# Kernel tuning notes

Hardware: AMD Instinct MI355X
Metric: run time of the kernel (lower is better)

## Reference

```python
import jax, jax.numpy as jnp
import numpy as np

N_PLACE = 100000
N_TRANS = 100000
E = 1000000
F_IN = 128
F_OUT = 64
H = 4
D = F_OUT // H
NEG_SLOPE = 0.2
EPS = 1e-16


def setup_inputs() -> dict:
    key = jax.random.key(0)
    ks = jax.random.split(key, 24)

    def rn(i, shape, s=1.0):
        return jax.random.normal(ks[i], shape, jnp.float32) * s

    def ei(i):
        k1, k2 = jax.random.split(ks[i])
        src = jax.random.randint(k1, (E,), 0, N_PLACE)
        dst = jax.random.randint(k2, (E,), 0, N_PLACE)
        return jnp.stack([src, dst]).astype(jnp.int32)

    return dict(
        x_place=rn(0, (N_PLACE, F_IN)),
        x_trans=rn(1, (N_TRANS, F_IN)),
        W_place=rn(2, (F_IN, F_OUT), 0.1),
        b_place=jnp.zeros((F_OUT,), jnp.float32),
        W_trans=rn(3, (F_IN, F_OUT), 0.1),
        b_trans=jnp.zeros((F_OUT,), jnp.float32),
        as_pt=rn(4, (H, D), 0.1), ad_pt=rn(5, (H, D), 0.1),
        as_tp=rn(6, (H, D), 0.1), ad_tp=rn(7, (H, D), 0.1),
        as_pp=rn(8, (H, D), 0.1), ad_pp=rn(9, (H, D), 0.1),
        as_tt=rn(10, (H, D), 0.1), ad_tt=rn(11, (H, D), 0.1),
        q=rn(12, (F_OUT,), 0.1),
        kW=rn(13, (F_OUT, F_OUT), 0.1),
        kb=jnp.zeros((F_OUT,), jnp.float32),
        ei_pt=ei(14), ei_tp=ei(15), ei_pp=ei(16), ei_tt=ei(17),
    )


def _rel(x_src, x_dst, ei, a_src, a_dst, n_dst):
    # Per-relation GAT-style attention (HANConv inner step).
    # x_src: [N_src, H, D], x_dst: [N_dst, H, D], ei: [2, E]
    src, dst = ei[0], ei[1]
    al_s = jnp.einsum('nhd,hd->nh', x_src, a_src)  # [N_src, H]
    al_d = jnp.einsum('nhd,hd->nh', x_dst, a_dst)  # [N_dst, H]
    alpha = jax.nn.leaky_relu(al_s[src] + al_d[dst], NEG_SLOPE)  # [E, H]
    # segment softmax over incoming edges of each dst node
    m = jax.ops.segment_max(alpha, dst, num_segments=n_dst)  # [N_dst, H]
    e = jnp.exp(alpha - m[dst])
    s = jax.ops.segment_sum(e, dst, num_segments=n_dst)
    a = e / (s[dst] + EPS)  # [E, H]
    out = jax.ops.segment_sum(x_src[src] * a[:, :, None], dst, num_segments=n_dst)
    return jax.nn.relu(out.reshape(n_dst, H * D))


def _group(outs, q, kW, kb):
    # HANConv semantic attention across relations targeting one node type.
    out = jnp.stack(outs)  # [R, N, F]
    score = jnp.einsum('f,rf->r', q, jnp.tanh(out @ kW + kb).mean(axis=1))  # [R]
    attn = jax.nn.softmax(score)
    return jnp.einsum('r,rnf->nf', attn, out)


def reference(x_place, x_trans, W_place, b_place, W_trans, b_trans,
              as_pt, ad_pt, as_tp, ad_tp, as_pp, ad_pp, as_tt, ad_tt,
              q, kW, kb, ei_pt, ei_tp, ei_pp, ei_tt):
    hp = (x_place @ W_place + b_place).reshape(N_PLACE, H, D)
    ht = (x_trans @ W_trans + b_trans).reshape(N_TRANS, H, D)
    out_t_pt = _rel(hp, ht, ei_pt, as_pt, ad_pt, N_TRANS)
    out_t_tt = _rel(ht, ht, ei_tt, as_tt, ad_tt, N_TRANS)
    out_p_tp = _rel(ht, hp, ei_tp, as_tp, ad_tp, N_PLACE)
    out_p_pp = _rel(hp, hp, ei_pp, as_pp, ad_pp, N_PLACE)
    out_place = _group([out_p_tp, out_p_pp], q, kW, kb)
    out_trans = _group([out_t_pt, out_t_tt], q, kW, kb)
    return out_place, out_trans
```

## Files before the change

kernel.cpp:

```cpp
#include <hip/hip_runtime.h>
#include <hip/hip_bf16.h>

#define NN 100000
#define NE 1000000
#define FI 128
#define FO 64
#define NB 196
#define CAP 8192
#define RELSTRIDE (256 * CAP)
#define TILE 4096
#define PROJ_T 512
#define PLACE_BLOCKS 128
#define ALB 128

typedef unsigned short u16;
typedef unsigned int u32;
typedef __attribute__((ext_vector_type(8))) short short8t;
typedef __attribute__((ext_vector_type(4))) float float4t;

__device__ __forceinline__ float bf2f(u16 u) {
    return __uint_as_float(((u32)u) << 16);
}
__device__ __forceinline__ u16 f2bf(float f) {
    __hip_bfloat16 h = __float2bfloat16(f);
    return *(u16*)&h;
}

__global__ __launch_bounds__(256) void init_kernel(int* __restrict__ bcursor,
                                                   float* __restrict__ mean_acc)
{
    const int rel = blockIdx.x;
    const int tid = threadIdx.x;
    bcursor[rel * 256 + tid] = tid * CAP;
    if (tid < 64) mean_acc[rel * 64 + tid] = 0.f;
}

__global__ __launch_bounds__(256) void phase1_kernel(
    const float* __restrict__ x_p, const float* __restrict__ W_p, const float* __restrict__ b_p,
    const float* __restrict__ x_t, const float* __restrict__ W_t, const float* __restrict__ b_t,
    u16* __restrict__ hb_place, u16* __restrict__ hb_trans,
    const int* __restrict__ ei_pt, const int* __restrict__ ei_tt,
    const int* __restrict__ ei_tp, const int* __restrict__ ei_pp,
    int* __restrict__ bcursor, u32* __restrict__ packed)
{
    __shared__ int smem[512];
    const int bid = blockIdx.x;
    const int tid = threadIdx.x;

    if (bid < 2 * PROJ_T) {
        const int ty = (bid >= PROJ_T);
        const float* __restrict__ x = ty ? x_t : x_p;
        const float* __restrict__ W = ty ? W_t : W_p;
        const float* __restrict__ b = ty ? b_t : b_p;
        u16* __restrict__ hout = ty ? hb_trans : hb_place;

        const int lane = tid & 63;
        const int wv   = tid >> 6;
        const int g    = lane >> 4;
        const int lo   = lane & 15;
        const int wid  = ((bid & (PROJ_T - 1)) << 2) | wv;

        short8t wf[4][4];
#pragma unroll
        for (int s = 0; s < 4; ++s)
#pragma unroll
            for (int t = 0; t < 4; ++t)
#pragma unroll
                for (int j = 0; j < 8; ++j)
                    wf[s][t][j] = (short)f2bf(W[(s * 32 + g * 8 + j) * FO + t * 16 + lo]);

        float bias[4];
#pragma unroll
        for (int t = 0; t < 4; ++t) bias[t] = b[t * 16 + lo];

        for (int tile = wid; tile < NN / 16; tile += 2048) {
            const int n0 = tile * 16;
            float4t acc[4];
#pragma unroll
            for (int t = 0; t < 4; ++t) { acc[t][0] = 0.f; acc[t][1] = 0.f; acc[t][2] = 0.f; acc[t][3] = 0.f; }

#pragma unroll
            for (int s = 0; s < 4; ++s) {
                const float* __restrict__ xr = x + (size_t)(n0 + lo) * FI + s * 32 + g * 8;
                const float4 u = *(const float4*)xr;
                const float4 v = *(const float4*)(xr + 4);
                short8t af;
                af[0] = (short)f2bf(u.x); af[1] = (short)f2bf(u.y);
                af[2] = (short)f2bf(u.z); af[3] = (short)f2bf(u.w);
                af[4] = (short)f2bf(v.x); af[5] = (short)f2bf(v.y);
                af[6] = (short)f2bf(v.z); af[7] = (short)f2bf(v.w);
#pragma unroll
                for (int t = 0; t < 4; ++t)
                    acc[t] = __builtin_amdgcn_mfma_f32_16x16x32_bf16(af, wf[s][t], acc[t], 0, 0, 0);
            }

#pragma unroll
            for (int t = 0; t < 4; ++t)
#pragma unroll
                for (int j = 0; j < 4; ++j)
                    hout[(size_t)(n0 + g * 4 + j) * FO + t * 16 + lo] = f2bf(acc[t][j] + bias[t]);
        }
    } else {
        const int pb = bid - 2 * PROJ_T;
        const int rel = pb >> 7;
        const int bx  = pb & 127;
        const int* ei = (rel == 0) ? ei_pt : (rel == 1) ? ei_tt : (rel == 2) ? ei_tp : ei_pp;
        u32* pk = packed + (size_t)rel * RELSTRIDE;

        int* lh = smem;
        int* lb = smem + 256;

        const int ntiles = (NE + TILE - 1) / TILE;
        for (int tile = bx; tile < ntiles; tile += PLACE_BLOCKS) {
            const int t0 = tile * TILE;
            lh[tid] = 0;
            __syncthreads();

            int d[TILE / 256];
#pragma unroll
            for (int i = 0; i < TILE / 256; ++i) {
                const int idx = t0 + i * 256 + tid;
                d[i] = (idx < NE) ? ei[NE + idx] : -1;
                if (d[i] >= 0) atomicAdd(&lh[d[i] >> 9], 1);
            }
            __syncthreads();
            if (lh[tid]) lb[tid] = atomicAdd(&bcursor[rel * 256 + tid], lh[tid]);
            __syncthreads();
#pragma unroll
            for (int i = 0; i < TILE / 256; ++i) {
                const int idx = t0 + i * 256 + tid;
                if (d[i] >= 0) {
                    const int src = ei[idx];
                    const int slot = atomicAdd(&lb[d[i] >> 9], 1);
                    pk[slot] = ((u32)(d[i] & 511) << 17) | (u32)src;
                }
            }
            __syncthreads();
        }
    }
}

__global__ __launch_bounds__(256) void csr_build_al(
    const u32* __restrict__ packed, const int* __restrict__ bcursor,
    int2* __restrict__ ofp, int* __restrict__ perm,
    const u16* __restrict__ hb_place, const u16* __restrict__ hb_trans,
    const float* __restrict__ as_pt, const float* __restrict__ as_pp,
    const float* __restrict__ ad_tp, const float* __restrict__ ad_pp,
    const float* __restrict__ as_tp, const float* __restrict__ as_tt,
    const float* __restrict__ ad_pt, const float* __restrict__ ad_tt,
    float* __restrict__ al_place, float* __restrict__ al_trans)
{
    const int by = blockIdx.y;
    const int bx = blockIdx.x;
    const int tid = threadIdx.x;

    if (bx < NB) {
        const int rel = by;
        const int b = bx;
        const int base = b * CAP;
        const int cnt  = bcursor[rel * 256 + b] - base;
        const u32* pk = packed + (size_t)rel * RELSTRIDE + base;
        int2* of = ofp + (size_t)rel * NN;
        int* pm = perm + (size_t)rel * RELSTRIDE;

        __shared__ int h[512];
        __shared__ int cur[512];
        h[tid] = 0; h[tid + 256] = 0;
        __syncthreads();
        for (int i = tid; i < cnt; i += 256)
            atomicAdd(&h[pk[i] >> 17], 1);
        __syncthreads();
        const int o0 = h[tid], o1 = h[tid + 256];
        for (int off = 1; off < 512; off <<= 1) {
            const int a0 = (tid >= off) ? h[tid - off] : 0;
            const int a1 = (tid + 256 >= off) ? h[tid + 256 - off] : 0;
            __syncthreads();
            h[tid] += a0; h[tid + 256] += a1;
            __syncthreads();
        }
        const int e0 = base + h[tid] - o0;
        const int e1 = base + h[tid + 256] - o1;
        const int gd0 = b * 512 + tid;
        const int gd1 = gd0 + 256;
        if (gd0 < NN) of[gd0] = make_int2(e0, e0 + o0);
        if (gd1 < NN) of[gd1] = make_int2(e1, e1 + o1);
        cur[tid] = e0; cur[tid + 256] = e1;
        __syncthreads();
        for (int i = tid; i < cnt; i += 256) {
            const u32 e = pk[i];
            const int slot = atomicAdd(&cur[e >> 17], 1);
            pm[slot] = (int)(e & 0x1FFFFu);
        }
    } else {
        const int ab = bx - NB;
        const int type = by >> 1;
        const int part = by & 1;
        const u16* hb = type ? hb_trans : hb_place;
        float* al = type ? al_trans : al_place;
        const float* a0 = type ? as_tp : as_pt;
        const float* a1 = type ? as_tt : as_pp;
        const float* a2 = type ? ad_pt : ad_tp;
        const float* a3 = type ? ad_tt : ad_pp;

        const int lane = tid & 63;
        const int wv   = tid >> 6;
        const int head = lane >> 4;
        const float av0 = a0[lane];
        const float av1 = a1[lane];
        const float av2 = a2[lane];
        const float av3 = a3[lane];

        const int HN = NN / 2;
        const int nw = ALB * 4;
        for (int n = part * HN + ab * 4 + wv; n < (part + 1) * HN; n += nw) {
            const float hv = bf2f(hb[(size_t)n * FO + lane]);
            float p0 = hv * av0, p1 = hv * av1, p2 = hv * av2, p3 = hv * av3;
#pragma unroll
            for (int off = 1; off < 16; off <<= 1) {
                p0 += __shfl_xor(p0, off);
                p1 += __shfl_xor(p1, off);
                p2 += __shfl_xor(p2, off);
                p3 += __shfl_xor(p3, off);
            }
            if ((lane & 15) == 0) {
                al[0 * NN * 4 + n * 4 + head] = p0;
                al[1 * NN * 4 + n * 4 + head] = p1;
                al[2 * NN * 4 + n * 4 + head] = p2;
                al[3 * NN * 4 + n * 4 + head] = p3;
            }
        }
    }
}

#define EDGE4(pm_, als_, hb_, cc, advh_, num_, den_, head_, lane_)                                  \
    {                                                                                               \
        const int s0 = pm_[cc], s1 = pm_[cc + 1], s2 = pm_[cc + 2], s3 = pm_[cc + 3];               \
        const float4 v0 = *(const float4*)(als_ + (size_t)s0 * 4);                                  \
        const float4 v1 = *(const float4*)(als_ + (size_t)s1 * 4);                                  \
        const float4 v2 = *(const float4*)(als_ + (size_t)s2 * 4);                                  \
        const float4 v3 = *(const float4*)(als_ + (size_t)s3 * 4);                                  \
        float a0 = ((head_ == 0) ? v0.x : (head_ == 1) ? v0.y : (head_ == 2) ? v0.z : v0.w) + advh_;\
        float a1 = ((head_ == 0) ? v1.x : (head_ == 1) ? v1.y : (head_ == 2) ? v1.z : v1.w) + advh_;\
        float a2 = ((head_ == 0) ? v2.x : (head_ == 1) ? v2.y : (head_ == 2) ? v2.z : v2.w) + advh_;\
        float a3 = ((head_ == 0) ? v3.x : (head_ == 1) ? v3.y : (head_ == 2) ? v3.z : v3.w) + advh_;\
        a0 = a0 > 0.f ? a0 : 0.2f * a0;                                                             \
        a1 = a1 > 0.f ? a1 : 0.2f * a1;                                                             \
        a2 = a2 > 0.f ? a2 : 0.2f * a2;                                                             \
        a3 = a3 > 0.f ? a3 : 0.2f * a3;                                                             \
        const float e0 = __expf(a0), e1 = __expf(a1), e2 = __expf(a2), e3 = __expf(a3);             \
        const float h0 = bf2f(hb_[(size_t)s0 * FO + lane_]);                                        \
        const float h1 = bf2f(hb_[(size_t)s1 * FO + lane_]);                                        \
        const float h2 = bf2f(hb_[(size_t)s2 * FO + lane_]);                                        \
        const float h3 = bf2f(hb_[(size_t)s3 * FO + lane_]);                                        \
        num_ = fmaf(h0, e0, num_);                                                                  \
        num_ = fmaf(h1, e1, num_);                                                                  \
        num_ = fmaf(h2, e2, num_);                                                                  \
        num_ = fmaf(h3, e3, num_);                                                                  \
        den_ += (e0 + e1) + (e2 + e3);                                                              \
    }

#define EDGE1(pm_, als_, hb_, cc, advh_, num_, den_, head_, lane_)                                  \
    {                                                                                               \
        const int s0 = pm_[cc];                                                                     \
        const float4 v0 = *(const float4*)(als_ + (size_t)s0 * 4);                                  \
        float a0 = ((head_ == 0) ? v0.x : (head_ == 1) ? v0.y : (head_ == 2) ? v0.z : v0.w) + advh_;\
        a0 = a0 > 0.f ? a0 : 0.2f * a0;                                                             \
        const float e0 = __expf(a0);                                                                \
        const float h0 = bf2f(hb_[(size_t)s0 * FO + lane_]);                                        \
        num_ = fmaf(h0, e0, num_);                                                                  \
        den_ += e0;                                                                                 \
    }

__global__ __launch_bounds__(256) void acc_kernel(
    const u16* __restrict__ hb_place, const u16* __restrict__ hb_trans,
    const float* __restrict__ al_place, const float* __restrict__ al_trans,
    const int2* __restrict__ ofp, const int* __restrict__ perm,
    u16* __restrict__ outb)
{
    const int rel = blockIdx.y;
    const u16* hb; const float* als; const float* ald;
    if (rel == 0)      { hb = hb_place; als = al_place + 0 * NN * 4; ald = al_trans + 2 * NN * 4; }
    else if (rel == 1) { hb = hb_trans; als = al_trans + 1 * NN * 4; ald = al_trans + 3 * NN * 4; }
    else if (rel == 2) { hb = hb_trans; als = al_trans + 0 * NN * 4; ald = al_place + 2 * NN * 4; }
    else               { hb = hb_place; als = al_place + 1 * NN * 4; ald = al_place + 3 * NN * 4; }
    const int2* of = ofp + (size_t)rel * NN;
    const int* pm = perm + (size_t)rel * RELSTRIDE;
    u16* ob = outb + (size_t)rel * NN * FO;

    const int lane = threadIdx.x & 63;
    const int wid  = threadIdx.x >> 6;
    const int head = lane >> 4;

    const int gw = blockIdx.x * 4 + wid;
    const int nw = gridDim.x * 4;
    for (int n = gw; n < NN; n += 2 * nw) {
        const int n2 = n + nw;
        const int nu = __builtin_amdgcn_readfirstlane(n);
        const int2 be = of[nu];
        int c1 = be.x;
        const int end1 = be.y;
        const float advh1 = ald[nu * 4 + head];
        float num1 = 0.f, den1 = 0.f;

        if (n2 < NN) {
            const int nu2 = __builtin_amdgcn_readfirstlane(n2);
            const int2 be2 = of[nu2];
            int c2 = be2.x;
            const int end2 = be2.y;
            const float advh2 = ald[nu2 * 4 + head];
            float num2 = 0.f, den2 = 0.f;

            while (c1 + 4 <= end1 && c2 + 4 <= end2) {
                EDGE4(pm, als, hb, c1, advh1, num1, den1, head, lane);
                EDGE4(pm, als, hb, c2, advh2, num2, den2, head, lane);
                c1 += 4; c2 += 4;
            }
            for (; c1 + 4 <= end1; c1 += 4) EDGE4(pm, als, hb, c1, advh1, num1, den1, head, lane);
            for (; c1 < end1; ++c1)         EDGE1(pm, als, hb, c1, advh1, num1, den1, head, lane);
            for (; c2 + 4 <= end2; c2 += 4) EDGE4(pm, als, hb, c2, advh2, num2, den2, head, lane);
            for (; c2 < end2; ++c2)         EDGE1(pm, als, hb, c2, advh2, num2, den2, head, lane);

            const float outv1 = fmaxf(num1 / (den1 + 1e-16f), 0.f);
            const float outv2 = fmaxf(num2 / (den2 + 1e-16f), 0.f);
            ob[(size_t)nu * FO + lane]  = f2bf(outv1);
            ob[(size_t)nu2 * FO + lane] = f2bf(outv2);
        } else {
            for (; c1 + 4 <= end1; c1 += 4) EDGE4(pm, als, hb, c1, advh1, num1, den1, head, lane);
            for (; c1 < end1; ++c1)         EDGE1(pm, als, hb, c1, advh1, num1, den1, head, lane);
            const float outv1 = fmaxf(num1 / (den1 + 1e-16f), 0.f);
            ob[(size_t)nu * FO + lane] = f2bf(outv1);
        }
    }
}

__global__ __launch_bounds__(256) void sem_kernel(
    const u16* __restrict__ outb, const float* __restrict__ kW, const float* __restrict__ kb,
    float* __restrict__ mean_acc)
{
    const int rel = blockIdx.y;
    const u16* ob = outb + (size_t)rel * NN * FO;
    const int QN = NN / 4;

    const int lane = threadIdx.x & 63;
    const int wid  = threadIdx.x >> 6;

    float kwc[FO];
#pragma unroll
    for (int k = 0; k < FO; ++k) kwc[k] = kW[k * FO + lane];
    const float kbv = kb[lane];

    float ts = 0.f;
    const int gw = blockIdx.x * 4 + wid;
    const int nw = gridDim.x * 4;
    for (int n = gw; n < QN; n += nw) {
        const int r0 = __builtin_amdgcn_readfirstlane(n);
        const int r1 = r0 + QN;
        const int r2 = r0 + 2 * QN;
        const int r3 = r0 + 3 * QN;
        const u32* w0 = (const u32*)(ob + (size_t)r0 * FO);
        const u32* w1 = (const u32*)(ob + (size_t)r1 * FO);
        const u32* w2 = (const u32*)(ob + (size_t)r2 * FO);
        const u32* w3 = (const u32*)(ob + (size_t)r3 * FO);
        float y0 = kbv, y1 = kbv, y2 = kbv, y3 = kbv;
#pragma unroll
        for (int i = 0; i < 32; ++i) {
            const u32 a = w0[i], b = w1[i], c = w2[i], d = w3[i];
            y0 = fmaf(__uint_as_float(a << 16),         kwc[2 * i],     y0);
            y0 = fmaf(__uint_as_float(a & 0xffff0000u), kwc[2 * i + 1], y0);
            y1 = fmaf(__uint_as_float(b << 16),         kwc[2 * i],     y1);
            y1 = fmaf(__uint_as_float(b & 0xffff0000u), kwc[2 * i + 1], y1);
            y2 = fmaf(__uint_as_float(c << 16),         kwc[2 * i],     y2);
            y2 = fmaf(__uint_as_float(c & 0xffff0000u), kwc[2 * i + 1], y2);
            y3 = fmaf(__uint_as_float(d << 16),         kwc[2 * i],     y3);
            y3 = fmaf(__uint_as_float(d & 0xffff0000u), kwc[2 * i + 1], y3);
        }
        ts += (tanhf(y0) + tanhf(y1)) + (tanhf(y2) + tanhf(y3));
    }

    __shared__ float red[4][64];
    red[wid][lane] = ts;
    __syncthreads();
    if (wid == 0) {
        const float sum = red[0][lane] + red[1][lane] + red[2][lane] + red[3][lane];
        unsafeAtomicAdd(&mean_acc[rel * 64 + lane], sum);
    }
}

__global__ __launch_bounds__(256) void combine_kernel(
    const u16* __restrict__ outb, const float* __restrict__ mean_acc,
    const float* __restrict__ q, float* __restrict__ out)
{
    const int lane = threadIdx.x & 63;
    const int type = blockIdx.y;
    const int r0i = (type == 0) ? 2 : 0;

    const float qv = q[lane];
    float s0 = qv * mean_acc[r0i * 64 + lane] * (1.0f / (float)NN);
    float s1 = qv * mean_acc[(r0i + 1) * 64 + lane] * (1.0f / (float)NN);
#pragma unroll
    for (int off = 1; off < 64; off <<= 1) {
        s0 += __shfl_xor(s0, off);
        s1 += __shfl_xor(s1, off);
    }
    const float m = fmaxf(s0, s1);
    const float e0 = expf(s0 - m), e1 = expf(s1 - m);
    const float a0 = e0 / (e0 + e1);
    const float a1 = e1 / (e0 + e1);

    const ushort4* o0 = (const ushort4*)(outb + (size_t)r0i * NN * FO);
    const ushort4* o1 = (const ushort4*)(outb + (size_t)(r0i + 1) * NN * FO);
    float4* dst = (float4*)(out + (size_t)type * NN * FO);
    const int n4 = NN * FO / 4;
    const int stride = gridDim.x * 256;
    for (int i = blockIdx.x * 256 + threadIdx.x; i < n4; i += stride) {
        const ushort4 u = o0[i];
        const ushort4 w = o1[i];
        float4 r;
        r.x = a0 * bf2f(u.x) + a1 * bf2f(w.x);
        r.y = a0 * bf2f(u.y) + a1 * bf2f(w.y);
        r.z = a0 * bf2f(u.z) + a1 * bf2f(w.z);
        r.w = a0 * bf2f(u.w) + a1 * bf2f(w.w);
        dst[i] = r;
    }
}

extern "C" void kernel_launch(void* const* d_in, const int* in_sizes, int n_in,
                              void* d_out, int out_size, void* d_ws, size_t ws_size,
                              hipStream_t stream)
{
    const float* x_place = (const float*)d_in[0];
    const float* x_trans = (const float*)d_in[1];
    const float* W_place = (const float*)d_in[2];
    const float* b_place = (const float*)d_in[3];
    const float* W_trans = (const float*)d_in[4];
    const float* b_trans = (const float*)d_in[5];
    const float* as_pt = (const float*)d_in[6];
    const float* ad_pt = (const float*)d_in[7];
    const float* as_tp = (const float*)d_in[8];
    const float* ad_tp = (const float*)d_in[9];
    const float* as_pp = (const float*)d_in[10];
    const float* ad_pp = (const float*)d_in[11];
    const float* as_tt = (const float*)d_in[12];
    const float* ad_tt = (const float*)d_in[13];
    const float* q  = (const float*)d_in[14];
    const float* kW = (const float*)d_in[15];
    const float* kb = (const float*)d_in[16];
    const int* ei_pt = (const int*)d_in[17];
    const int* ei_tp = (const int*)d_in[18];
    const int* ei_pp = (const int*)d_in[19];
    const int* ei_tt = (const int*)d_in[20];

    char* ws = (char*)d_ws;
    u16* hb_place = (u16*)ws;
    u16* hb_trans = hb_place + (size_t)NN * FO;
    float* al_place = (float*)(hb_trans + (size_t)NN * FO);
    float* al_trans = al_place + 4 * (size_t)NN * 4;
    u16* outb = (u16*)(al_trans + 4 * (size_t)NN * 4);
    int2* ofp = (int2*)(outb + 4 * (size_t)NN * FO);
    int* perm = (int*)(ofp + 4 * (size_t)NN);
    u32* packed = (u32*)(perm + 4 * (size_t)RELSTRIDE);
    int* bcursor = (int*)(packed + 4 * (size_t)RELSTRIDE);
    float* mean_acc = (float*)(bcursor + 4 * 256);

    init_kernel<<<4, 256, 0, stream>>>(bcursor, mean_acc);

    phase1_kernel<<<2 * PROJ_T + 4 * PLACE_BLOCKS, 256, 0, stream>>>(
        x_place, W_place, b_place,
        x_trans, W_trans, b_trans,
        hb_place, hb_trans,
        ei_pt, ei_tt, ei_tp, ei_pp, bcursor, packed);

    csr_build_al<<<dim3(NB + ALB, 4), 256, 0, stream>>>(
        packed, bcursor, ofp, perm,
        hb_place, hb_trans,
        as_pt, as_pp, ad_tp, ad_pp,
        as_tp, as_tt, ad_pt, ad_tt,
        al_place, al_trans);

    acc_kernel<<<dim3(1024, 4), 256, 0, stream>>>(hb_place, hb_trans, al_place, al_trans,
                                                  ofp, perm, outb);

    sem_kernel<<<dim3(512, 4), 256, 0, stream>>>(outb, kW, kb, mean_acc);

    combine_kernel<<<dim3(1024, 2), 256, 0, stream>>>(outb, mean_acc, q, (float*)d_out);
}
```

Baseline: 462.6 us.

## Fuse attention logits into projection and precompute per-edge exp weights in CSR build

The per-node attention logits are now computed inside the projection MFMA epilogue from the fp32 accumulators, which removes the separate logit pass that re-read the bf16 features. The CSR build kernel now gathers source and destination logits per edge, applies leaky-relu and exp, and stores bf16 weights aligned with the permutation array. The accumulation kernel then reads those weights instead of doing random float4 gathers and exponentials. This trades extra writes and reads of an 8-byte-per-edge weight array for removing gathers from the hot loop, adds bf16 rounding of the unnormalized exp values, and lowers CAP to 6144, which leaves less headroom for per-bucket overflow.

```diff
diff --git a/kernel.cpp b/kernel.cpp
--- a/kernel.cpp
+++ b/kernel.cpp
@@ -6,12 +6,11 @@
 #define FI 128
 #define FO 64
 #define NB 196
-#define CAP 8192
+#define CAP 6144
 #define RELSTRIDE (256 * CAP)
 #define TILE 4096
 #define PROJ_T 512
 #define PLACE_BLOCKS 128
-#define ALB 128
 
 typedef unsigned short u16;
 typedef unsigned int u32;
@@ -37,8 +36,13 @@
 
 __global__ __launch_bounds__(256) void phase1_kernel(
     const float* __restrict__ x_p, const float* __restrict__ W_p, const float* __restrict__ b_p,
+    const float* __restrict__ p_a0, const float* __restrict__ p_a1,
+    const float* __restrict__ p_a2, const float* __restrict__ p_a3,
     const float* __restrict__ x_t, const float* __restrict__ W_t, const float* __restrict__ b_t,
+    const float* __restrict__ t_a0, const float* __restrict__ t_a1,
+    const float* __restrict__ t_a2, const float* __restrict__ t_a3,
     u16* __restrict__ hb_place, u16* __restrict__ hb_trans,
+    float* __restrict__ al_place, float* __restrict__ al_trans,
     const int* __restrict__ ei_pt, const int* __restrict__ ei_tt,
     const int* __restrict__ ei_tp, const int* __restrict__ ei_pp,
     int* __restrict__ bcursor, u32* __restrict__ packed)
@@ -52,7 +56,12 @@
         const float* __restrict__ x = ty ? x_t : x_p;
         const float* __restrict__ W = ty ? W_t : W_p;
         const float* __restrict__ b = ty ? b_t : b_p;
+        const float* a0 = ty ? t_a0 : p_a0;
+        const float* a1 = ty ? t_a1 : p_a1;
+        const float* a2 = ty ? t_a2 : p_a2;
+        const float* a3 = ty ? t_a3 : p_a3;
         u16* __restrict__ hout = ty ? hb_trans : hb_place;
+        float* __restrict__ al = ty ? al_trans : al_place;
 
         const int lane = tid & 63;
         const int wv   = tid >> 6;
@@ -72,6 +81,15 @@
         float bias[4];
 #pragma unroll
         for (int t = 0; t < 4; ++t) bias[t] = b[t * 16 + lo];
+
+        float avv[4][4];
+#pragma unroll
+        for (int t = 0; t < 4; ++t) {
+            avv[0][t] = a0[t * 16 + lo];
+            avv[1][t] = a1[t * 16 + lo];
+            avv[2][t] = a2[t * 16 + lo];
+            avv[3][t] = a3[t * 16 + lo];
+        }
 
         for (int tile = wid; tile < NN / 16; tile += 2048) {
             const int n0 = tile * 16;
@@ -99,6 +117,21 @@
 #pragma unroll
                 for (int j = 0; j < 4; ++j)
                     hout[(size_t)(n0 + g * 4 + j) * FO + t * 16 + lo] = f2bf(acc[t][j] + bias[t]);
+
+#pragma unroll
+            for (int m = 0; m < 4; ++m)
+#pragma unroll
+                for (int t = 0; t < 4; ++t)
+#pragma unroll
+                    for (int j = 0; j < 4; ++j) {
+                        float p = (acc[t][j] + bias[t]) * avv[m][t];
+                        p += __shfl_xor(p, 1);
+                        p += __shfl_xor(p, 2);
+                        p += __shfl_xor(p, 4);
+                        p += __shfl_xor(p, 8);
+                        if (lo == 0)
+                            al[(size_t)m * NN * 4 + (size_t)(n0 + g * 4 + j) * 4 + t] = p;
+                    }
         }
     } else {
         const int pb = bid - 2 * PROJ_T;
@@ -140,114 +173,80 @@
     }
 }
 
-__global__ __launch_bounds__(256) void csr_build_al(
+__global__ __launch_bounds__(256) void csr_build(
     const u32* __restrict__ packed, const int* __restrict__ bcursor,
-    int2* __restrict__ ofp, int* __restrict__ perm,
-    const u16* __restrict__ hb_place, const u16* __restrict__ hb_trans,
-    const float* __restrict__ as_pt, const float* __restrict__ as_pp,
-    const float* __restrict__ ad_tp, const float* __restrict__ ad_pp,
-    const float* __restrict__ as_tp, const float* __restrict__ as_tt,
-    const float* __restrict__ ad_pt, const float* __restrict__ ad_tt,
-    float* __restrict__ al_place, float* __restrict__ al_trans)
-{
-    const int by = blockIdx.y;
-    const int bx = blockIdx.x;
+    int2* __restrict__ ofp, int* __restrict__ perm, ushort4* __restrict__ pal,
+    const float* __restrict__ al_place, const float* __restrict__ al_trans)
+{
+    const int rel = blockIdx.y;
+    const int b = blockIdx.x;
     const int tid = threadIdx.x;
-
-    if (bx < NB) {
-        const int rel = by;
-        const int b = bx;
-        const int base = b * CAP;
-        const int cnt  = bcursor[rel * 256 + b] - base;
-        const u32* pk = packed + (size_t)rel * RELSTRIDE + base;
-        int2* of = ofp + (size_t)rel * NN;
-        int* pm = perm + (size_t)rel * RELSTRIDE;
-
-        __shared__ int h[512];
-        __shared__ int cur[512];
-        h[tid] = 0; h[tid + 256] = 0;
+    const int base = b * CAP;
+    const int cnt  = bcursor[rel * 256 + b] - base;
+    const u32* pk = packed + (size_t)rel * RELSTRIDE + base;
+    int2* of = ofp + (size_t)rel * NN;
+    int* pm = perm + (size_t)rel * RELSTRIDE;
+    ushort4* pw = pal + (size_t)rel * RELSTRIDE;
+
+    const float* als; const float* ald;
+    if (rel == 0)      { als = al_place + 0 * NN * 4; ald = al_trans + 2 * NN * 4; }
+    else if (rel == 1) { als = al_trans + 1 * NN * 4; ald = al_trans + 3 * NN * 4; }
+    else if (rel == 2) { als = al_trans + 0 * NN * 4; ald = al_place + 2 * NN * 4; }
+    else               { als = al_place + 1 * NN * 4; ald = al_place + 3 * NN * 4; }
+
+    __shared__ int h[512];
+    __shared__ int cur[512];
+    h[tid] = 0; h[tid + 256] = 0;
+    __syncthreads();
+    for (int i = tid; i < cnt; i += 256)
+        atomicAdd(&h[pk[i] >> 17], 1);
+    __syncthreads();
+    const int o0 = h[tid], o1 = h[tid + 256];
+    for (int off = 1; off < 512; off <<= 1) {
+        const int a0 = (tid >= off) ? h[tid - off] : 0;
+        const int a1 = (tid + 256 >= off) ? h[tid + 256 - off] : 0;
         __syncthreads();
-        for (int i = tid; i < cnt; i += 256)
-            atomicAdd(&h[pk[i] >> 17], 1);
+        h[tid] += a0; h[tid + 256] += a1;
         __syncthreads();
-        const int o0 = h[tid], o1 = h[tid + 256];
-        for (int off = 1; off < 512; off <<= 1) {
-            const int a0 = (tid >= off) ? h[tid - off] : 0;
-            const int a1 = (tid + 256 >= off) ? h[tid + 256 - off] : 0;
-            __syncthreads();
-            h[tid] += a0; h[tid + 256] += a1;
-            __syncthreads();
-        }
-        const int e0 = base + h[tid] - o0;
-        const int e1 = base + h[tid + 256] - o1;
-        const int gd0 = b * 512 + tid;
-        const int gd1 = gd0 + 256;
-        if (gd0 < NN) of[gd0] = make_int2(e0, e0 + o0);
-        if (gd1 < NN) of[gd1] = make_int2(e1, e1 + o1);
-        cur[tid] = e0; cur[tid + 256] = e1;
-        __syncthreads();
-        for (int i = tid; i < cnt; i += 256) {
-            const u32 e = pk[i];
-            const int slot = atomicAdd(&cur[e >> 17], 1);
-            pm[slot] = (int)(e & 0x1FFFFu);
-        }
-    } else {
-        const int ab = bx - NB;
-        const int type = by >> 1;
-        const int part = by & 1;
-        const u16* hb = type ? hb_trans : hb_place;
-        float* al = type ? al_trans : al_place;
-        const float* a0 = type ? as_tp : as_pt;
-        const float* a1 = type ? as_tt : as_pp;
-        const float* a2 = type ? ad_pt : ad_tp;
-        const float* a3 = type ? ad_tt : ad_pp;
-
-        const int lane = tid & 63;
-        const int wv   = tid >> 6;
-        const int head = lane >> 4;
-        const float av0 = a0[lane];
-        const float av1 = a1[lane];
-        const float av2 = a2[lane];
-        const float av3 = a3[lane];
-
-        const int HN = NN / 2;
-        const int nw = ALB * 4;
-        for (int n = part * HN + ab * 4 + wv; n < (part + 1) * HN; n += nw) {
-            const float hv = bf2f(hb[(size_t)n * FO + lane]);
-            float p0 = hv * av0, p1 = hv * av1, p2 = hv * av2, p3 = hv * av3;
-#pragma unroll
-            for (int off = 1; off < 16; off <<= 1) {
-                p0 += __shfl_xor(p0, off);
-                p1 += __shfl_xor(p1, off);
-                p2 += __shfl_xor(p2, off);
-                p3 += __shfl_xor(p3, off);
-            }
-            if ((lane & 15) == 0) {
-                al[0 * NN * 4 + n * 4 + head] = p0;
-                al[1 * NN * 4 + n * 4 + head] = p1;
-                al[2 * NN * 4 + n * 4 + head] = p2;
-                al[3 * NN * 4 + n * 4 + head] = p3;
-            }
-        }
-    }
-}
-
-#define EDGE4(pm_, als_, hb_, cc, advh_, num_, den_, head_, lane_)                                  \
+    }
+    const int e0 = base + h[tid] - o0;
+    const int e1 = base + h[tid + 256] - o1;
+    const int gd0 = b * 512 + tid;
+    const int gd1 = gd0 + 256;
+    if (gd0 < NN) of[gd0] = make_int2(e0, e0 + o0);
+    if (gd1 < NN) of[gd1] = make_int2(e1, e1 + o1);
+    cur[tid] = e0; cur[tid + 256] = e1;
+    __syncthreads();
+    for (int i = tid; i < cnt; i += 256) {
+        const u32 e = pk[i];
+        const int src = (int)(e & 0x1FFFFu);
+        const int dl  = (int)(e >> 17);
+        const int slot = atomicAdd(&cur[dl], 1);
+        const int gd = b * 512 + dl;
+        const float4 va = *(const float4*)(als + (size_t)src * 4);
+        const float4 vd = *(const float4*)(ald + (size_t)gd * 4);
+        float a0 = va.x + vd.x; a0 = a0 > 0.f ? a0 : 0.2f * a0;
+        float a1 = va.y + vd.y; a1 = a1 > 0.f ? a1 : 0.2f * a1;
+        float a2 = va.z + vd.z; a2 = a2 > 0.f ? a2 : 0.2f * a2;
+        float a3 = va.w + vd.w; a3 = a3 > 0.f ? a3 : 0.2f * a3;
+        ushort4 w;
+        w.x = f2bf(__expf(a0));
+        w.y = f2bf(__expf(a1));
+        w.z = f2bf(__expf(a2));
+        w.w = f2bf(__expf(a3));
+        pm[slot] = src;
+        pw[slot] = w;
+    }
+}
+
+#define EDGE4(pm_, pw_, hb_, cc, num_, den_, head_, lane_)                                          \
     {                                                                                               \
         const int s0 = pm_[cc], s1 = pm_[cc + 1], s2 = pm_[cc + 2], s3 = pm_[cc + 3];               \
-        const float4 v0 = *(const float4*)(als_ + (size_t)s0 * 4);                                  \
-        const float4 v1 = *(const float4*)(als_ + (size_t)s1 * 4);                                  \
-        const float4 v2 = *(const float4*)(als_ + (size_t)s2 * 4);                                  \
-        const float4 v3 = *(const float4*)(als_ + (size_t)s3 * 4);                                  \
-        float a0 = ((head_ == 0) ? v0.x : (head_ == 1) ? v0.y : (head_ == 2) ? v0.z : v0.w) + advh_;\
-        float a1 = ((head_ == 0) ? v1.x : (head_ == 1) ? v1.y : (head_ == 2) ? v1.z : v1.w) + advh_;\
-        float a2 = ((head_ == 0) ? v2.x : (head_ == 1) ? v2.y : (head_ == 2) ? v2.z : v2.w) + advh_;\
-        float a3 = ((head_ == 0) ? v3.x : (head_ == 1) ? v3.y : (head_ == 2) ? v3.z : v3.w) + advh_;\
-        a0 = a0 > 0.f ? a0 : 0.2f * a0;                                                             \
-        a1 = a1 > 0.f ? a1 : 0.2f * a1;                                                             \
-        a2 = a2 > 0.f ? a2 : 0.2f * a2;                                                             \
-        a3 = a3 > 0.f ? a3 : 0.2f * a3;                                                             \
-        const float e0 = __expf(a0), e1 = __expf(a1), e2 = __expf(a2), e3 = __expf(a3);             \
+        const ushort4 q0 = pw_[cc], q1 = pw_[cc + 1], q2 = pw_[cc + 2], q3 = pw_[cc + 3];           \
+        const float e0 = bf2f((head_ == 0) ? q0.x : (head_ == 1) ? q0.y : (head_ == 2) ? q0.z : q0.w);\
+        const float e1 = bf2f((head_ == 0) ? q1.x : (head_ == 1) ? q1.y : (head_ == 2) ? q1.z : q1.w);\
+        const float e2 = bf2f((head_ == 0) ? q2.x : (head_ == 1) ? q2.y : (head_ == 2) ? q2.z : q2.w);\
+        const float e3 = bf2f((head_ == 0) ? q3.x : (head_ == 1) ? q3.y : (head_ == 2) ? q3.z : q3.w);\
         const float h0 = bf2f(hb_[(size_t)s0 * FO + lane_]);                                        \
         const float h1 = bf2f(hb_[(size_t)s1 * FO + lane_]);                                        \
         const float h2 = bf2f(hb_[(size_t)s2 * FO + lane_]);                                        \
@@ -259,13 +258,11 @@
         den_ += (e0 + e1) + (e2 + e3);                                                              \
     }
 
-#define EDGE1(pm_, als_, hb_, cc, advh_, num_, den_, head_, lane_)                                  \
+#define EDGE1(pm_, pw_, hb_, cc, num_, den_, head_, lane_)                                          \
     {                                                                                               \
         const int s0 = pm_[cc];                                                                     \
-        const float4 v0 = *(const float4*)(als_ + (size_t)s0 * 4);                                  \
-        float a0 = ((head_ == 0) ? v0.x : (head_ == 1) ? v0.y : (head_ == 2) ? v0.z : v0.w) + advh_;\
-        a0 = a0 > 0.f ? a0 : 0.2f * a0;                                                             \
-        const float e0 = __expf(a0);                                                                \
+        const ushort4 q0 = pw_[cc];                                                                 \
+        const float e0 = bf2f((head_ == 0) ? q0.x : (head_ == 1) ? q0.y : (head_ == 2) ? q0.z : q0.w);\
         const float h0 = bf2f(hb_[(size_t)s0 * FO + lane_]);                                        \
         num_ = fmaf(h0, e0, num_);                                                                  \
         den_ += e0;                                                                                 \
@@ -273,18 +270,14 @@
 
 __global__ __launch_bounds__(256) void acc_kernel(
     const u16* __restrict__ hb_place, const u16* __restrict__ hb_trans,
-    const float* __restrict__ al_place, const float* __restrict__ al_trans,
     const int2* __restrict__ ofp, const int* __restrict__ perm,
-    u16* __restrict__ outb)
+    const ushort4* __restrict__ pal, u16* __restrict__ outb)
 {
     const int rel = blockIdx.y;
-    const u16* hb; const float* als; const float* ald;
-    if (rel == 0)      { hb = hb_place; als = al_place + 0 * NN * 4; ald = al_trans + 2 * NN * 4; }
-    else if (rel == 1) { hb = hb_trans; als = al_trans + 1 * NN * 4; ald = al_trans + 3 * NN * 4; }
-    else if (rel == 2) { hb = hb_trans; als = al_trans + 0 * NN * 4; ald = al_place + 2 * NN * 4; }
-    else               { hb = hb_place; als = al_place + 1 * NN * 4; ald = al_place + 3 * NN * 4; }
+    const u16* hb = (rel == 0 || rel == 3) ? hb_place : hb_trans;
     const int2* of = ofp + (size_t)rel * NN;
     const int* pm = perm + (size_t)rel * RELSTRIDE;
+    const ushort4* pw = pal + (size_t)rel * RELSTRIDE;
     u16* ob = outb + (size_t)rel * NN * FO;
 
     const int lane = threadIdx.x & 63;
@@ -299,7 +292,6 @@
         const int2 be = of[nu];
         int c1 = be.x;
         const int end1 = be.y;
-        const float advh1 = ald[nu * 4 + head];
         float num1 = 0.f, den1 = 0.f;
 
         if (n2 < NN) {
@@ -307,26 +299,25 @@
             const int2 be2 = of[nu2];
             int c2 = be2.x;
             const int end2 = be2.y;
-            const float advh2 = ald[nu2 * 4 + head];
             float num2 = 0.f, den2 = 0.f;
 
             while (c1 + 4 <= end1 && c2 + 4 <= end2) {
-                EDGE4(pm, als, hb, c1, advh1, num1, den1, head, lane);
-                EDGE4(pm, als, hb, c2, advh2, num2, den2, head, lane);
+                EDGE4(pm, pw, hb, c1, num1, den1, head, lane);
+                EDGE4(pm, pw, hb, c2, num2, den2, head, lane);
                 c1 += 4; c2 += 4;
             }
-            for (; c1 + 4 <= end1; c1 += 4) EDGE4(pm, als, hb, c1, advh1, num1, den1, head, lane);
-            for (; c1 < end1; ++c1)         EDGE1(pm, als, hb, c1, advh1, num1, den1, head, lane);
-            for (; c2 + 4 <= end2; c2 += 4) EDGE4(pm, als, hb, c2, advh2, num2, den2, head, lane);
-            for (; c2 < end2; ++c2)         EDGE1(pm, als, hb, c2, advh2, num2, den2, head, lane);
+            for (; c1 + 4 <= end1; c1 += 4) EDGE4(pm, pw, hb, c1, num1, den1, head, lane);
+            for (; c1 < end1; ++c1)         EDGE1(pm, pw, hb, c1, num1, den1, head, lane);
+            for (; c2 + 4 <= end2; c2 += 4) EDGE4(pm, pw, hb, c2, num2, den2, head, lane);
+            for (; c2 < end2; ++c2)         EDGE1(pm, pw, hb, c2, num2, den2, head, lane);
 
             const float outv1 = fmaxf(num1 / (den1 + 1e-16f), 0.f);
             const float outv2 = fmaxf(num2 / (den2 + 1e-16f), 0.f);
             ob[(size_t)nu * FO + lane]  = f2bf(outv1);
             ob[(size_t)nu2 * FO + lane] = f2bf(outv2);
         } else {
-            for (; c1 + 4 <= end1; c1 += 4) EDGE4(pm, als, hb, c1, advh1, num1, den1, head, lane);
-            for (; c1 < end1; ++c1)         EDGE1(pm, als, hb, c1, advh1, num1, den1, head, lane);
+            for (; c1 + 4 <= end1; c1 += 4) EDGE4(pm, pw, hb, c1, num1, den1, head, lane);
+            for (; c1 < end1; ++c1)         EDGE1(pm, pw, hb, c1, num1, den1, head, lane);
             const float outv1 = fmaxf(num1 / (den1 + 1e-16f), 0.f);
             ob[(size_t)nu * FO + lane] = f2bf(outv1);
         }
@@ -459,26 +450,22 @@
     int2* ofp = (int2*)(outb + 4 * (size_t)NN * FO);
     int* perm = (int*)(ofp + 4 * (size_t)NN);
     u32* packed = (u32*)(perm + 4 * (size_t)RELSTRIDE);
-    int* bcursor = (int*)(packed + 4 * (size_t)RELSTRIDE);
+    ushort4* pal = (ushort4*)(packed + 4 * (size_t)RELSTRIDE);
+    int* bcursor = (int*)(pal + 4 * (size_t)RELSTRIDE);
     float* mean_acc = (float*)(bcursor + 4 * 256);
 
     init_kernel<<<4, 256, 0, stream>>>(bcursor, mean_acc);
 
     phase1_kernel<<<2 * PROJ_T + 4 * PLACE_BLOCKS, 256, 0, stream>>>(
-        x_place, W_place, b_place,
-        x_trans, W_trans, b_trans,
-        hb_place, hb_trans,
+        x_place, W_place, b_place, as_pt, as_pp, ad_tp, ad_pp,
+        x_trans, W_trans, b_trans, as_tp, as_tt, ad_pt, ad_tt,
+        hb_place, hb_trans, al_place, al_trans,
         ei_pt, ei_tt, ei_tp, ei_pp, bcursor, packed);
 
-    csr_build_al<<<dim3(NB + ALB, 4), 256, 0, stream>>>(
-        packed, bcursor, ofp, perm,
-        hb_place, hb_trans,
-        as_pt, as_pp, ad_tp, ad_pp,
-        as_tp, as_tt, ad_pt, ad_tt,
-        al_place, al_trans);
-
-    acc_kernel<<<dim3(1024, 4), 256, 0, stream>>>(hb_place, hb_trans, al_place, al_trans,
-                                                  ofp, perm, outb);
+    csr_build<<<dim3(NB, 4), 256, 0, stream>>>(packed, bcursor, ofp, perm, pal,
+                                               al_place, al_trans);
+
+    acc_kernel<<<dim3(1024, 4), 256, 0, stream>>>(hb_place, hb_trans, ofp, perm, pal, outb);
 
     sem_kernel<<<dim3(512, 4), 256, 0, stream>>>(outb, kW, kb, mean_acc);
 
```

New measurement: 551.8 us. +19.3%, slower.
